# Kernel optimization log

Measured on AMD Instinct MI355X. Metric: run time of the kernel, lower is better.

## Reference

```python
import jax, jax.numpy as jnp
import numpy as np

# Scale constants (production tokenizer-style)
P = 1_048_576   # total flat byte-params (sum of token lengths over vocab)
E = 8_388_608   # occurrence edges: (token-instance, byte-within-token) pairs
T = 4_194_304   # text length in bytes
N = 2_097_152   # number of token instances (valid_tokens)
INIT_STD = 0.02


def setup_inputs() -> dict:
    key = jax.random.key(0)
    k1, k2, k3, k4 = jax.random.split(key, 4)
    flat_params = jax.random.normal(k1, (P,), dtype=jnp.float32) * INIT_STD
    # occ_param_idx[e] = offset[token_id_e] + byte_idx_e  (index into flat param vector)
    occ_param_idx = jax.random.randint(k2, (E,), 0, P, dtype=jnp.int32)
    # occ_byte_pos[e] = start_pos_e + byte_idx_e  (absolute byte position in text)
    occ_byte_pos = jax.random.randint(k3, (E,), 0, T, dtype=jnp.int32)
    # occ_token_idx[e] = which token instance this byte occurrence belongs to
    occ_token_idx = jax.random.randint(k4, (E,), 0, N, dtype=jnp.int32)
    return {
        "flat_params": flat_params,
        "occ_param_idx": occ_param_idx,
        "occ_byte_pos": occ_byte_pos,
        "occ_token_idx": occ_token_idx,
        "text_len": T,
        "num_tokens": N,
    }


def reference(flat_params, occ_param_idx, occ_byte_pos, occ_token_idx, text_len, num_tokens):
    # 1) gather per-occurrence byte params
    vals = flat_params[occ_param_idx]                                      # [E]
    # 2) scatter-add into byte positions: sum and count per byte
    byte_sum = jax.ops.segment_sum(vals, occ_byte_pos, num_segments=text_len)            # [T]
    byte_cnt = jax.ops.segment_sum(jnp.ones_like(vals), occ_byte_pos, num_segments=text_len)  # [T]
    # 3) mean per byte (0 where no token covers the byte, as in the torch code)
    byte_w = jnp.where(byte_cnt > 0, byte_sum / jnp.maximum(byte_cnt, 1.0), 0.0)          # [T]
    # 4) each token's position = sum of byte weights over its span
    positions = jax.ops.segment_sum(byte_w[occ_byte_pos], occ_token_idx, num_segments=num_tokens)  # [N]
    return positions
```

## Files before the change

### kernel.cpp

```cpp
#include <hip/hip_runtime.h>


typedef unsigned long long u64;
typedef unsigned int uint;

constexpr int NB   = 512;
constexpr int PPB  = 8192;
constexpr int NB2  = 512;
constexpr int TOKB = 4096;
constexpr int CAP  = 17408;
constexpr int CAP2 = 17408;

constexpr float V_SCALE = 2097152.0f;
constexpr float V_INV   = 1.0f / 2097152.0f;
constexpr float W_SCALE = 1048576.0f;
constexpr float W_INV   = 1.0f / 1048576.0f;

__device__ __forceinline__ void scan512(const uint* hist, uint* scn,
                                        uint* lbase, int t) {
    if (t < 512) scn[t] = hist[t];
    __syncthreads();
    #pragma unroll
    for (int step = 1; step < 512; step <<= 1) {
        uint v = 0;
        if (t < 512) { v = scn[t]; if (t >= step) v += scn[t - step]; }
        __syncthreads();
        if (t < 512) scn[t] = v;
        __syncthreads();
    }
    if (t < 512) lbase[t] = scn[t] - hist[t];
    if (t == 0)  lbase[512] = scn[511];
    __syncthreads();
}

__device__ __forceinline__ int find_bucket512(const uint* lbase, uint i) {
    int lo = 0, hi = 511;
    while (lo < hi) {
        int mid = (lo + hi) >> 1;
        if (lbase[mid + 1] <= i) lo = mid + 1; else hi = mid;
    }
    return lo;
}

constexpr int A_THREADS = 1024;
constexpr int A_EPT     = 8;
constexpr int A_CHUNK   = A_THREADS * A_EPT;

__global__ __launch_bounds__(A_THREADS) void phaseA(
    const float* __restrict__ fp, const int* __restrict__ pidx,
    const int* __restrict__ bpos, const int* __restrict__ tidx,
    u64* __restrict__ recs, uint* __restrict__ gcur, int E)
{
    __shared__ u64 stage[A_CHUNK];
    __shared__ uint hist[NB], lcur[NB], gbase[NB];
    __shared__ uint scn[NB], lbase[NB + 1];
    int t = threadIdx.x;
    if (t < NB) { hist[t] = 0u; lcur[t] = 0u; }
    __syncthreads();

    int start = blockIdx.x * A_CHUNK;
    int base_e = start + t * A_EPT;
    bool vec = (base_e + A_EPT) <= E;

    float v0=0,v1=0,v2=0,v3=0,v4=0,v5=0,v6=0,v7=0;
    if (vec) {
        int4 p0 = *(const int4*)(pidx + base_e);
        int4 p1 = *(const int4*)(pidx + base_e + 4);
        v0 = fp[p0.x]; v1 = fp[p0.y]; v2 = fp[p0.z]; v3 = fp[p0.w];
        v4 = fp[p1.x]; v5 = fp[p1.y]; v6 = fp[p1.z]; v7 = fp[p1.w];
        int4 b0 = *(const int4*)(bpos + base_e);
        int4 b1 = *(const int4*)(bpos + base_e + 4);
        atomicAdd(&hist[((uint)b0.x) >> 13], 1u);
        atomicAdd(&hist[((uint)b0.y) >> 13], 1u);
        atomicAdd(&hist[((uint)b0.z) >> 13], 1u);
        atomicAdd(&hist[((uint)b0.w) >> 13], 1u);
        atomicAdd(&hist[((uint)b1.x) >> 13], 1u);
        atomicAdd(&hist[((uint)b1.y) >> 13], 1u);
        atomicAdd(&hist[((uint)b1.z) >> 13], 1u);
        atomicAdd(&hist[((uint)b1.w) >> 13], 1u);
    } else {
        for (int j = 0; j < A_EPT; ++j) {
            int e = base_e + j;
            if (e < E) atomicAdd(&hist[((uint)bpos[e]) >> 13], 1u);
        }
    }
    __syncthreads();
    scan512(hist, scn, lbase, t);
    if (t < NB) gbase[t] = atomicAdd(&gcur[t], hist[t]);
    __syncthreads();

    auto emit = [&](int p, int tk, float v) {
        uint b = ((uint)p) >> 13;
        int fx = (int)rintf(v * V_SCALE);
        u64 rec = (u64)(uint)(p & (PPB - 1))
                | ((u64)(uint)tk << 13)
                | ((u64)(uint)(fx + (1 << 20)) << 34)
                | ((u64)b << 55);
        uint off = lbase[b] + atomicAdd(&lcur[b], 1u);
        stage[off] = rec;
    };
    if (vec) {
        int4 b0 = *(const int4*)(bpos + base_e);
        int4 b1 = *(const int4*)(bpos + base_e + 4);
        int4 k0 = *(const int4*)(tidx + base_e);
        int4 k1 = *(const int4*)(tidx + base_e + 4);
        emit(b0.x, k0.x, v0); emit(b0.y, k0.y, v1);
        emit(b0.z, k0.z, v2); emit(b0.w, k0.w, v3);
        emit(b1.x, k1.x, v4); emit(b1.y, k1.y, v5);
        emit(b1.z, k1.z, v6); emit(b1.w, k1.w, v7);
    } else {
        for (int j = 0; j < A_EPT; ++j) {
            int e = base_e + j;
            if (e < E) emit(bpos[e], tidx[e], fp[pidx[e]]);
        }
    }
    __syncthreads();

    uint total = lbase[NB];
    for (uint i = t; i < total; i += A_THREADS) {
        u64 rc = stage[i];
        int b = (int)(rc >> 55);
        uint dst = gbase[b] + (i - lbase[b]);
        if (dst < (uint)CAP)
            recs[(size_t)b * CAP + dst] = rc;
    }
}

constexpr int C_THREADS = 1024;
constexpr int C_CHUNK   = 8192;
constexpr int C_MAXCH   = (CAP + C_CHUNK - 1) / C_CHUNK;

__global__ __launch_bounds__(C_THREADS) void phaseC(
    const u64* __restrict__ recs, const uint* __restrict__ gcur,
    uint* __restrict__ rec2, uint* __restrict__ gcur2)
{
    __shared__ uint acc[PPB];
    __shared__ uint stage2[C_CHUNK];
    __shared__ uint histc[C_MAXCH][NB2];
    __shared__ uint lcur[NB2], gbase[NB2];
    __shared__ uint scn[NB2], lbase[NB2 + 1];
    int t = threadIdx.x;
    int b = blockIdx.x;
    for (int i = t; i < PPB; i += C_THREADS) acc[i] = 0u;
    for (int i = t; i < C_MAXCH * NB2; i += C_THREADS) (&histc[0][0])[i] = 0u;
    __syncthreads();

    uint n = min(gcur[b], (uint)CAP);
    const u64* r = recs + (size_t)b * CAP;

    auto process = [&](u64 rc, uint ch) {
        uint pos = (uint)rc & (PPB - 1);
        int fx = (int)((uint)(rc >> 34) & 0x1FFFFFu) - (1 << 20);
        atomicAdd(&acc[pos], (uint)((1 << 26) + fx));
        atomicAdd(&histc[ch][(uint)(rc >> 25) & 0x1FFu], 1u);
    };
    uint np = n >> 1;
    for (uint i = t; i < np; i += C_THREADS) {
        ulonglong2 rr = ((const ulonglong2*)r)[i];
        uint ch = (2u * i) / C_CHUNK;
        process(rr.x, ch); process(rr.y, ch);
    }
    for (uint i = 2u * np + t; i < n; i += C_THREADS) process(r[i], i / C_CHUNK);
    __syncthreads();

    uint ch = 0;
    for (uint c0 = 0; c0 < n; c0 += C_CHUNK, ++ch) {
        uint m = min((uint)C_CHUNK, n - c0);
        if (t < NB2) lcur[t] = 0u;
        __syncthreads();
        scan512(histc[ch], scn, lbase, t);
        if (t < NB2) gbase[t] = atomicAdd(&gcur2[t], histc[ch][t]);
        __syncthreads();
        for (uint i = t; i < m; i += C_THREADS) {
            u64 rc = r[c0 + i];
            uint pos = (uint)rc & (PPB - 1);
            uint tok = (uint)(rc >> 13) & 0x1FFFFFu;
            uint a = acc[pos];
            uint c = (a + (1u << 25)) >> 26;
            int s = (int)(a - (c << 26));
            float w = (float)s * V_INV / (float)c;
            int wfx = (int)rintf(w * W_SCALE);
            uint tb = tok >> 12;
            uint off = lbase[tb] + atomicAdd(&lcur[tb], 1u);
            stage2[off] = (tok & (TOKB - 1)) | ((uint)wfx << 12);
        }
        __syncthreads();
        uint total = lbase[NB2];
        for (uint i = t; i < total; i += C_THREADS) {
            int tb = find_bucket512(lbase, i);
            uint dst = gbase[tb] + (i - lbase[tb]);
            if (dst < (uint)CAP2)
                rec2[(size_t)tb * CAP2 + dst] = stage2[i];
        }
        __syncthreads();
    }
}

constexpr int D_THREADS = 1024;

__global__ __launch_bounds__(D_THREADS) void phaseD(
    const uint* __restrict__ rec2, const uint* __restrict__ gcur2,
    float* __restrict__ out, int N)
{
    __shared__ int facc[TOKB];
    int t = threadIdx.x;
    int b = blockIdx.x;
    for (int i = t; i < TOKB; i += D_THREADS) facc[i] = 0;
    __syncthreads();
    uint n = min(gcur2[b], (uint)CAP2);
    const uint* r = rec2 + (size_t)b * CAP2;
    uint nq = n >> 2;
    for (uint i = t; i < nq; i += D_THREADS) {
        uint4 q = ((const uint4*)r)[i];
        atomicAdd(&facc[q.x & (TOKB - 1)], ((int)q.x) >> 12);
        atomicAdd(&facc[q.y & (TOKB - 1)], ((int)q.y) >> 12);
        atomicAdd(&facc[q.z & (TOKB - 1)], ((int)q.z) >> 12);
        atomicAdd(&facc[q.w & (TOKB - 1)], ((int)q.w) >> 12);
    }
    for (uint i = 4u * nq + t; i < n; i += D_THREADS) {
        uint rc = r[i];
        atomicAdd(&facc[rc & (TOKB - 1)], ((int)rc) >> 12);
    }
    __syncthreads();
    int base = b * TOKB;
    for (int i = t; i < TOKB; i += D_THREADS) {
        int idx = base + i;
        if (idx < N) out[idx] = (float)facc[i] * W_INV;
    }
}

__global__ void fb_scatter(const float* __restrict__ fp,
                           const int* __restrict__ pidx,
                           const int* __restrict__ bpos,
                           u64* __restrict__ bacc, int E) {
    int e = blockIdx.x * blockDim.x + threadIdx.x;
    if (e < E) {
        float v = fp[pidx[e]];
        long long fx = (long long)rintf(v * 4294967296.0f);
        atomicAdd(&bacc[bpos[e]], (1ULL << 39) + (u64)fx);
    }
}

__global__ void fb_tokens(const u64* __restrict__ bacc,
                          const int* __restrict__ bpos,
                          const int* __restrict__ tidx,
                          float* __restrict__ out, int E) {
    int e = blockIdx.x * blockDim.x + threadIdx.x;
    if (e < E) {
        u64 v = bacc[bpos[e]];
        long long cnt = (long long)((v + (1ULL << 38)) >> 39);
        long long s   = (long long)(v - ((u64)cnt << 39));
        atomicAdd(&out[tidx[e]], (float)s * (1.0f / 4294967296.0f) / (float)cnt);
    }
}

extern "C" void kernel_launch(void* const* d_in, const int* in_sizes, int n_in,
                              void* d_out, int out_size, void* d_ws, size_t ws_size,
                              hipStream_t stream) {
    const float* flat_params   = (const float*)d_in[0];
    const int*   occ_param_idx = (const int*)d_in[1];
    const int*   occ_byte_pos  = (const int*)d_in[2];
    const int*   occ_token_idx = (const int*)d_in[3];

    const int E = in_sizes[1];
    const int N = out_size;

    const size_t REC_BYTES  = (size_t)NB  * CAP  * 8;
    const size_t REC2_BYTES = (size_t)NB2 * CAP2 * 4;
    const size_t NEED = 4096 + REC_BYTES + REC2_BYTES;

    if (ws_size >= NEED && N <= NB2 * TOKB) {
        uint* gcur  = (uint*)d_ws;
        uint* gcur2 = (uint*)((char*)d_ws + 2048);
        u64* recs = (u64*)((char*)d_ws + 4096);
        uint* rec2 = (uint*)((char*)d_ws + 4096 + REC_BYTES);

        hipMemsetAsync(d_ws, 0, 4096, stream);

        int gridA = (E + A_CHUNK - 1) / A_CHUNK;
        phaseA<<<gridA, A_THREADS, 0, stream>>>(flat_params, occ_param_idx,
                                                occ_byte_pos, occ_token_idx,
                                                recs, gcur, E);
        phaseC<<<NB, C_THREADS, 0, stream>>>(recs, gcur, rec2, gcur2);
        phaseD<<<NB2, D_THREADS, 0, stream>>>(rec2, gcur2, (float*)d_out, N);
    } else {
        u64* bacc = (u64*)d_ws;
        hipMemsetAsync(bacc, 0, (size_t)4194304 * 8, stream);
        hipMemsetAsync(d_out, 0, (size_t)N * sizeof(float), stream);
        int gridE = (E + 255) / 256;
        fb_scatter<<<gridE, 256, 0, stream>>>(flat_params, occ_param_idx,
                                              occ_byte_pos, bacc, E);
        fb_tokens<<<gridE, 256, 0, stream>>>(bacc, occ_byte_pos,
                                             occ_token_idx, (float*)d_out, E);
    }
}
```

Measured before the change: 272.5 us.

## Replace block-wide scans with wavefront shuffle scan and per-bucket wave scatter

```diff
diff --git a/kernel.cpp b/kernel.cpp
--- a/kernel.cpp
+++ b/kernel.cpp
@@ -16,30 +16,24 @@
 constexpr float W_SCALE = 1048576.0f;
 constexpr float W_INV   = 1.0f / 1048576.0f;
 
-__device__ __forceinline__ void scan512(const uint* hist, uint* scn,
-                                        uint* lbase, int t) {
-    if (t < 512) scn[t] = hist[t];
-    __syncthreads();
-    #pragma unroll
-    for (int step = 1; step < 512; step <<= 1) {
-        uint v = 0;
-        if (t < 512) { v = scn[t]; if (t >= step) v += scn[t - step]; }
-        __syncthreads();
-        if (t < 512) scn[t] = v;
-        __syncthreads();
-    }
-    if (t < 512) lbase[t] = scn[t] - hist[t];
-    if (t == 0)  lbase[512] = scn[511];
-    __syncthreads();
-}
-
-__device__ __forceinline__ int find_bucket512(const uint* lbase, uint i) {
-    int lo = 0, hi = 511;
-    while (lo < hi) {
-        int mid = (lo + hi) >> 1;
-        if (lbase[mid + 1] <= i) lo = mid + 1; else hi = mid;
-    }
-    return lo;
+__device__ __forceinline__ void wave_scan512(const uint* hist, uint* lbase,
+                                             int t) {
+    if (t < 64) {
+        uint h[8];
+        uint run = 0;
+        #pragma unroll
+        for (int j = 0; j < 8; ++j) { h[j] = run; run += hist[t * 8 + j]; }
+        uint tot = run, inc = tot;
+        #pragma unroll
+        for (int d = 1; d < 64; d <<= 1) {
+            uint up = __shfl_up(inc, d, 64);
+            if (t >= d) inc += up;
+        }
+        uint excl = inc - tot;
+        #pragma unroll
+        for (int j = 0; j < 8; ++j) lbase[t * 8 + j] = excl + h[j];
+        if (t == 63) lbase[512] = inc;
+    }
 }
 
 constexpr int A_THREADS = 1024;
@@ -52,24 +46,25 @@
     u64* __restrict__ recs, uint* __restrict__ gcur, int E)
 {
     __shared__ u64 stage[A_CHUNK];
-    __shared__ uint hist[NB], lcur[NB], gbase[NB];
-    __shared__ uint scn[NB], lbase[NB + 1];
+    __shared__ uint hist[NB], lcur[NB], gbase[NB], lbase[NB + 1];
     int t = threadIdx.x;
     if (t < NB) { hist[t] = 0u; lcur[t] = 0u; }
     __syncthreads();
 
-    int start = blockIdx.x * A_CHUNK;
-    int base_e = start + t * A_EPT;
+    int base_e = blockIdx.x * A_CHUNK + t * A_EPT;
     bool vec = (base_e + A_EPT) <= E;
 
+    int4 b0, b1, k0, k1;
     float v0=0,v1=0,v2=0,v3=0,v4=0,v5=0,v6=0,v7=0;
     if (vec) {
         int4 p0 = *(const int4*)(pidx + base_e);
         int4 p1 = *(const int4*)(pidx + base_e + 4);
+        b0 = *(const int4*)(bpos + base_e);
+        b1 = *(const int4*)(bpos + base_e + 4);
+        k0 = *(const int4*)(tidx + base_e);
+        k1 = *(const int4*)(tidx + base_e + 4);
         v0 = fp[p0.x]; v1 = fp[p0.y]; v2 = fp[p0.z]; v3 = fp[p0.w];
         v4 = fp[p1.x]; v5 = fp[p1.y]; v6 = fp[p1.z]; v7 = fp[p1.w];
-        int4 b0 = *(const int4*)(bpos + base_e);
-        int4 b1 = *(const int4*)(bpos + base_e + 4);
         atomicAdd(&hist[((uint)b0.x) >> 13], 1u);
         atomicAdd(&hist[((uint)b0.y) >> 13], 1u);
         atomicAdd(&hist[((uint)b0.z) >> 13], 1u);
@@ -85,8 +80,9 @@
         }
     }
     __syncthreads();
-    scan512(hist, scn, lbase, t);
-    if (t < NB) gbase[t] = atomicAdd(&gcur[t], hist[t]);
+
+    wave_scan512(hist, lbase, t);
+    if (t >= 512) gbase[t - 512] = atomicAdd(&gcur[t - 512], hist[t - 512]);
     __syncthreads();
 
     auto emit = [&](int p, int tk, float v) {
@@ -100,10 +96,6 @@
         stage[off] = rec;
     };
     if (vec) {
-        int4 b0 = *(const int4*)(bpos + base_e);
-        int4 b1 = *(const int4*)(bpos + base_e + 4);
-        int4 k0 = *(const int4*)(tidx + base_e);
-        int4 k1 = *(const int4*)(tidx + base_e + 4);
         emit(b0.x, k0.x, v0); emit(b0.y, k0.y, v1);
         emit(b0.z, k0.z, v2); emit(b0.w, k0.w, v3);
         emit(b1.x, k1.x, v4); emit(b1.y, k1.y, v5);
@@ -137,12 +129,12 @@
     __shared__ uint acc[PPB];
     __shared__ uint stage2[C_CHUNK];
     __shared__ uint histc[C_MAXCH][NB2];
-    __shared__ uint lcur[NB2], gbase[NB2];
-    __shared__ uint scn[NB2], lbase[NB2 + 1];
+    __shared__ uint lcur[NB2], gb[NB2], lbase[NB2 + 1];
     int t = threadIdx.x;
     int b = blockIdx.x;
     for (int i = t; i < PPB; i += C_THREADS) acc[i] = 0u;
     for (int i = t; i < C_MAXCH * NB2; i += C_THREADS) (&histc[0][0])[i] = 0u;
+    if (t < NB2) lcur[t] = 0u;
     __syncthreads();
 
     uint n = min(gcur[b], (uint)CAP);
@@ -163,13 +155,18 @@
     for (uint i = 2u * np + t; i < n; i += C_THREADS) process(r[i], i / C_CHUNK);
     __syncthreads();
 
+    if (t >= 512) {
+        int tb = t - 512;
+        uint tot = histc[0][tb];
+        #pragma unroll
+        for (int c = 1; c < C_MAXCH; ++c) tot += histc[c][tb];
+        gb[tb] = atomicAdd(&gcur2[tb], tot);
+    }
+
     uint ch = 0;
     for (uint c0 = 0; c0 < n; c0 += C_CHUNK, ++ch) {
         uint m = min((uint)C_CHUNK, n - c0);
-        if (t < NB2) lcur[t] = 0u;
-        __syncthreads();
-        scan512(histc[ch], scn, lbase, t);
-        if (t < NB2) gbase[t] = atomicAdd(&gcur2[t], histc[ch][t]);
+        wave_scan512(histc[ch], lbase, t);
         __syncthreads();
         for (uint i = t; i < m; i += C_THREADS) {
             u64 rc = r[c0 + i];
@@ -185,13 +182,19 @@
             stage2[off] = (tok & (TOKB - 1)) | ((uint)wfx << 12);
         }
         __syncthreads();
-        uint total = lbase[NB2];
-        for (uint i = t; i < total; i += C_THREADS) {
-            int tb = find_bucket512(lbase, i);
-            uint dst = gbase[tb] + (i - lbase[tb]);
-            if (dst < (uint)CAP2)
-                rec2[(size_t)tb * CAP2 + dst] = stage2[i];
-        }
+        int w = t >> 6, lane = t & 63;
+        for (int tb = w; tb < NB2; tb += 16) {
+            uint base = lbase[tb];
+            uint len  = lbase[tb + 1] - base;
+            uint g    = gb[tb];
+            for (uint j = lane; j < len; j += 64) {
+                uint dst = g + j;
+                if (dst < (uint)CAP2)
+                    rec2[(size_t)tb * CAP2 + dst] = stage2[base + j];
+            }
+        }
+        __syncthreads();
+        if (t < NB2) { gb[t] += histc[ch][t]; lcur[t] = 0u; }
         __syncthreads();
     }
 }
```

New measurement: 265.1 us. 2.7% less time.
